# Kernel tuning notes

Hardware: AMD Instinct MI355X
Metric: run time of the kernel (lower is better)

Reference implementation:

```python
import jax, jax.numpy as jnp
import numpy as np

B, N, D = 8, 4096, 3
MAX_K = 16


def setup_inputs() -> dict:
    key = jax.random.key(0)
    k1, k2, k3 = jax.random.split(key, 3)
    x = jax.random.normal(k1, (B, N, D), dtype=jnp.float32)
    preds = jax.random.normal(k2, (B, N, D), dtype=jnp.float32)
    k_vector = jax.random.normal(k3, (MAX_K,), dtype=jnp.float32)  # learned param
    return {"x": x, "preds": preds, "k_vector": k_vector}


def _pairwise_dist(x):
    # Euclidean cdist via ||a||^2 + ||b||^2 - 2 a.b, avoiding a [B,N,N,D] tensor.
    sq = jnp.sum(x * x, axis=-1)                      # [B, N]
    inner = jnp.einsum('bnd,bmd->bnm', x, x)          # [B, N, N]
    d2 = sq[:, :, None] + sq[:, None, :] - 2.0 * inner
    return jnp.sqrt(jnp.maximum(d2, 0.0))             # [B, N, N]


def reference(x, preds, k_vector):
    # k = argmax(softmax(k_vector)) + 1 ; softmax is monotone so argmax suffices.
    # In the torch original .item() makes k a Python int (static w.r.t. the graph).
    k = int(np.asarray(jnp.argmax(k_vector))) + 1

    dist = _pairwise_dist(x)                          # [B, N, N]
    # torch.topk(..., largest=False): k smallest distances -> top_k of negated.
    _, idx = jax.lax.top_k(-dist, k)                  # idx: [B, N, k]

    # Gather predicted coords of the k nearest neighbors per point.
    b_idx = jnp.arange(preds.shape[0])[:, None, None]  # [B,1,1]
    knn_coords = preds[b_idx, idx]                     # [B, N, k, D]
    new_space = jnp.mean(knn_coords, axis=2)           # [B, N, D]
    return new_space
```

## Files before the change

kernel.cpp:

```cpp
#include <hip/hip_runtime.h>
#include <math.h>

typedef unsigned long long u64;
typedef unsigned int u32;

#define BB 8
#define NN 4096
#define MAXK 16
#define BQ 64
#define BUFSLOTS 16


__device__ __forceinline__ void bitonic16(u64 v[MAXK]) {
#pragma unroll
    for (int k = 2; k <= 16; k <<= 1) {
#pragma unroll
        for (int j = k >> 1; j > 0; j >>= 1) {
#pragma unroll
            for (int i = 0; i < 16; ++i) {
                const int l = i ^ j;
                if (l > i) {
                    const u64 a = v[i], b = v[l];
                    const bool up = ((i & k) == 0);
                    const bool sw = up ? (a > b) : (a < b);
                    v[i] = sw ? b : a;
                    v[l] = sw ? a : b;
                }
            }
        }
    }
}

__device__ __forceinline__ void merge16(u64 list[MAXK], const u64 br[MAXK]) {
    u64 lo[MAXK];
#pragma unroll
    for (int i = 0; i < 16; ++i) {
        const u64 a = list[i], b = br[15 - i];
        lo[i] = a < b ? a : b;
    }
#pragma unroll
    for (int j = 8; j > 0; j >>= 1) {
#pragma unroll
        for (int i = 0; i < 16; ++i) {
            const int l = i ^ j;
            if (l > i) {
                const u64 a = lo[i], b = lo[l];
                const bool sw = a > b;
                lo[i] = sw ? b : a;
                lo[l] = sw ? a : b;
            }
        }
    }
#pragma unroll
    for (int i = 0; i < 16; ++i) list[i] = lo[i];
}

__device__ __forceinline__ void flush_buf(u64 list[MAXK], u64& wkey, int& cnt,
                                          const u64 (*buf)[BQ], int lane) {
    u64 br[MAXK];
#pragma unroll
    for (int i = 0; i < 16; ++i) {
        const u64 v = buf[i][lane];
        br[i] = (i < cnt) ? v : ~0ull;
    }
    bitonic16(br);
    merge16(list, br);
    wkey = list[15];
    cnt = 0;
}

__device__ __forceinline__ void write_mean(const float* __restrict__ pb,
                                           const float* __restrict__ kvec,
                                           const u64 list[MAXK],
                                           float* __restrict__ op) {
    float bv = kvec[0]; int bi = 0;
#pragma unroll
    for (int i = 1; i < MAXK; ++i) { const float v = kvec[i]; if (v > bv) { bv = v; bi = i; } }
    const int k = bi + 1;
    float sx = 0.f, sy = 0.f, sz = 0.f;
#pragma unroll
    for (int s = 0; s < MAXK; ++s) {
        if (s < k) {
            const int j = (int)(u32)list[s];
            sx = __fadd_rn(sx, pb[j * 3 + 0]);
            sy = __fadd_rn(sy, pb[j * 3 + 1]);
            sz = __fadd_rn(sz, pb[j * 3 + 2]);
        }
    }
    const float fk = (float)k;
    op[0] = __fdiv_rn(sx, fk);
    op[1] = __fdiv_rn(sy, fk);
    op[2] = __fdiv_rn(sz, fk);
}

__global__ __launch_bounds__(256) void knn_prep(const float* __restrict__ x,
                                                float4* __restrict__ tab) {
    const int i = blockIdx.x * 256 + (int)threadIdx.x;
    const float cx = x[i * 3 + 0], cy = x[i * 3 + 1], cz = x[i * 3 + 2];
    const float sq = __fadd_rn(__fadd_rn(__fmul_rn(cx, cx), __fmul_rn(cy, cy)),
                               __fmul_rn(cz, cz));
    tab[i] = make_float4(cx, cy, cz, sq);
}

template <int SEGS, bool TAB, bool FUSED>
__global__ __launch_bounds__(BQ) void knn_scan(
    const float* __restrict__ x, const float* __restrict__ preds,
    const float* __restrict__ kvec, const float4* __restrict__ tab,
    u64* __restrict__ wkeys, float* __restrict__ out)
{
    constexpr int SEGLEN = NN / SEGS;
    int bid = blockIdx.x;
    const int seg = bid % SEGS;
    bid /= SEGS;
    const int qg = bid % (NN / BQ);
    const int b  = bid / (NN / BQ);
    const int lane = (int)threadIdx.x;
    const int qi = qg * BQ + lane;

    const float* xb = x + (size_t)b * NN * 3;
    const float4* tb = TAB ? (tab + (size_t)b * NN) : nullptr;

    float qx, qy, qz, qsq;
    if (TAB) {
        const float4 qv = tb[qi];
        qx = qv.x; qy = qv.y; qz = qv.z; qsq = qv.w;
    } else {
        qx = xb[qi * 3 + 0]; qy = xb[qi * 3 + 1]; qz = xb[qi * 3 + 2];
        qsq = __fadd_rn(__fadd_rn(__fmul_rn(qx, qx), __fmul_rn(qy, qy)),
                        __fmul_rn(qz, qz));
    }

    __shared__ u64 buf[BUFSLOTS][BQ];

    u64 list[MAXK];
#pragma unroll
    for (int s = 0; s < MAXK; ++s) list[s] = ~0ull;
    u64 wkey = ~0ull;
    int cnt = 0;

    const int jbase = seg * SEGLEN;
#pragma unroll 1
    for (int t = 0; t < SEGLEN; t += 4) {
        if (__any((int)(cnt > BUFSLOTS - 4))) flush_buf(list, wkey, cnt, buf, lane);
#pragma unroll
        for (int u = 0; u < 4; ++u) {
            const int j = jbase + t + u;
            float cx, cy, cz, csq;
            if (TAB) {
                const float4 c = tb[j];
                cx = c.x; cy = c.y; cz = c.z; csq = c.w;
            } else {
                cx = xb[j * 3 + 0]; cy = xb[j * 3 + 1]; cz = xb[j * 3 + 2];
                csq = __fadd_rn(__fadd_rn(__fmul_rn(cx, cx), __fmul_rn(cy, cy)),
                                __fmul_rn(cz, cz));
            }
            const float inner = __fadd_rn(
                __fadd_rn(__fmul_rn(qx, cx), __fmul_rn(qy, cy)),
                __fmul_rn(qz, cz));
            float d2 = __fsub_rn(__fadd_rn(qsq, csq), __fmul_rn(2.0f, inner));
            d2 = fmaxf(d2, 0.0f);
            const u64 key = ((u64)__float_as_uint(d2) << 32) | (u32)j;
            buf[cnt][lane] = key;
            cnt += (key < wkey) ? 1 : 0;
        }
    }
    flush_buf(list, wkey, cnt, buf, lane);

    if (FUSED) {
        write_mean(preds + (size_t)b * NN * 3, kvec, list,
                   out + ((size_t)b * NN + qi) * 3);
    } else {
        const size_t q = (size_t)b * NN + qi;
#pragma unroll
        for (int s = 0; s < MAXK; ++s)
            wkeys[(size_t)(seg * MAXK + s) * (BB * NN) + q] = list[s];
    }
}

template <int SEGS>
__global__ __launch_bounds__(BQ) void knn_merge(
    const float* __restrict__ preds, const float* __restrict__ kvec,
    const u64* __restrict__ wkeys, float* __restrict__ out)
{
    const int lane = (int)threadIdx.x;
    const int q = blockIdx.x * BQ + lane;

    __shared__ u64 buf[BUFSLOTS][BQ];

    u64 list[MAXK];
#pragma unroll
    for (int s = 0; s < MAXK; ++s) list[s] = ~0ull;
    u64 wkey = ~0ull;
    int cnt = 0;

#pragma unroll 1
    for (int i = 0; i < SEGS * MAXK; i += 4) {
        if (__any((int)(cnt > BUFSLOTS - 4))) flush_buf(list, wkey, cnt, buf, lane);
#pragma unroll
        for (int u = 0; u < 4; ++u) {
            const u64 key = wkeys[(size_t)(i + u) * (BB * NN) + q];
            buf[cnt][lane] = key;
            cnt += (key < wkey) ? 1 : 0;
        }
    }
    flush_buf(list, wkey, cnt, buf, lane);

    const int b = q / NN;
    write_mean(preds + (size_t)b * NN * 3, kvec, list, out + (size_t)q * 3);
}

extern "C" void kernel_launch(void* const* d_in, const int* in_sizes, int n_in,
                              void* d_out, int out_size, void* d_ws, size_t ws_size,
                              hipStream_t stream) {
    (void)in_sizes; (void)n_in; (void)out_size;
    const float* x     = (const float*)d_in[0];
    const float* preds = (const float*)d_in[1];
    const float* kvec  = (const float*)d_in[2];
    float* out = (float*)d_out;

    const size_t keys8 = 8ull * MAXK * BB * NN * sizeof(u64);
    const size_t keys4 = 4ull * MAXK * BB * NN * sizeof(u64);
    const size_t tabsz = (size_t)BB * NN * sizeof(float4);

    if (ws_size >= keys8 + tabsz) {
        u64* wkeys  = (u64*)d_ws;
        float4* tab = (float4*)((char*)d_ws + keys8);
        knn_prep<<<(BB * NN) / 256, 256, 0, stream>>>(x, tab);
        knn_scan<8, true, false><<<BB * (NN / BQ) * 8, BQ, 0, stream>>>(
            x, preds, kvec, tab, wkeys, out);
        knn_merge<8><<<(BB * NN) / BQ, BQ, 0, stream>>>(preds, kvec, wkeys, out);
    } else if (ws_size >= keys4 + tabsz) {
        u64* wkeys  = (u64*)d_ws;
        float4* tab = (float4*)((char*)d_ws + keys4);
        knn_prep<<<(BB * NN) / 256, 256, 0, stream>>>(x, tab);
        knn_scan<4, true, false><<<BB * (NN / BQ) * 4, BQ, 0, stream>>>(
            x, preds, kvec, tab, wkeys, out);
        knn_merge<4><<<(BB * NN) / BQ, BQ, 0, stream>>>(preds, kvec, wkeys, out);
    } else if (ws_size >= keys4) {
        u64* wkeys = (u64*)d_ws;
        knn_scan<4, false, false><<<BB * (NN / BQ) * 4, BQ, 0, stream>>>(
            x, preds, kvec, nullptr, wkeys, out);
        knn_merge<4><<<(BB * NN) / BQ, BQ, 0, stream>>>(preds, kvec, wkeys, out);
    } else {
        knn_scan<1, false, true><<<BB * (NN / BQ), BQ, 0, stream>>>(
            x, preds, kvec, nullptr, nullptr, out);
    }
}
```

Baseline: 158.5 us.

## Split KNN scan into 16 segments and merge sorted segment lists directly

The scan now splits candidates into 16 segments when the workspace allows, raising the number of blocks. The inner loop is unrolled to 8 candidates per buffer check. The prep table stores pre-doubled coordinates so the 2*inner multiply is dropped. The merge kernel runs with 256 threads and merges already-sorted 16-entry segment lists with merge16 instead of re-buffering and re-sorting every key. In exchange, the 16-way split writes and reads twice as many intermediate keys, and the larger buffer threshold causes more frequent flushes.

```diff
diff --git a/kernel.cpp b/kernel.cpp
--- a/kernel.cpp
+++ b/kernel.cpp
@@ -9,6 +9,7 @@
 #define MAXK 16
 #define BQ 64
 #define BUFSLOTS 16
+#define UNROLL 8
 
 
 __device__ __forceinline__ void bitonic16(u64 v[MAXK]) {
@@ -99,7 +100,8 @@
     const float cx = x[i * 3 + 0], cy = x[i * 3 + 1], cz = x[i * 3 + 2];
     const float sq = __fadd_rn(__fadd_rn(__fmul_rn(cx, cx), __fmul_rn(cy, cy)),
                                __fmul_rn(cz, cz));
-    tab[i] = make_float4(cx, cy, cz, sq);
+    tab[i] = make_float4(__fadd_rn(cx, cx), __fadd_rn(cy, cy),
+                         __fadd_rn(cz, cz), sq);
 }
 
 template <int SEGS, bool TAB, bool FUSED>
@@ -123,7 +125,10 @@
     float qx, qy, qz, qsq;
     if (TAB) {
         const float4 qv = tb[qi];
-        qx = qv.x; qy = qv.y; qz = qv.z; qsq = qv.w;
+        qx = __fmul_rn(0.5f, qv.x);
+        qy = __fmul_rn(0.5f, qv.y);
+        qz = __fmul_rn(0.5f, qv.z);
+        qsq = qv.w;
     } else {
         qx = xb[qi * 3 + 0]; qy = xb[qi * 3 + 1]; qz = xb[qi * 3 + 2];
         qsq = __fadd_rn(__fadd_rn(__fmul_rn(qx, qx), __fmul_rn(qy, qy)),
@@ -140,24 +145,25 @@
 
     const int jbase = seg * SEGLEN;
 #pragma unroll 1
-    for (int t = 0; t < SEGLEN; t += 4) {
-        if (__any((int)(cnt > BUFSLOTS - 4))) flush_buf(list, wkey, cnt, buf, lane);
-#pragma unroll
-        for (int u = 0; u < 4; ++u) {
+    for (int t = 0; t < SEGLEN; t += UNROLL) {
+        if (__any((int)(cnt > BUFSLOTS - UNROLL))) flush_buf(list, wkey, cnt, buf, lane);
+#pragma unroll
+        for (int u = 0; u < UNROLL; ++u) {
             const int j = jbase + t + u;
-            float cx, cy, cz, csq;
+            float c2x, c2y, c2z, csq;
             if (TAB) {
                 const float4 c = tb[j];
-                cx = c.x; cy = c.y; cz = c.z; csq = c.w;
+                c2x = c.x; c2y = c.y; c2z = c.z; csq = c.w;
             } else {
-                cx = xb[j * 3 + 0]; cy = xb[j * 3 + 1]; cz = xb[j * 3 + 2];
+                const float cx = xb[j * 3 + 0], cy = xb[j * 3 + 1], cz = xb[j * 3 + 2];
                 csq = __fadd_rn(__fadd_rn(__fmul_rn(cx, cx), __fmul_rn(cy, cy)),
                                 __fmul_rn(cz, cz));
+                c2x = __fadd_rn(cx, cx); c2y = __fadd_rn(cy, cy); c2z = __fadd_rn(cz, cz);
             }
-            const float inner = __fadd_rn(
-                __fadd_rn(__fmul_rn(qx, cx), __fmul_rn(qy, cy)),
-                __fmul_rn(qz, cz));
-            float d2 = __fsub_rn(__fadd_rn(qsq, csq), __fmul_rn(2.0f, inner));
+            const float inner2 = __fadd_rn(
+                __fadd_rn(__fmul_rn(qx, c2x), __fmul_rn(qy, c2y)),
+                __fmul_rn(qz, c2z));
+            float d2 = __fsub_rn(__fadd_rn(qsq, csq), inner2);
             d2 = fmaxf(d2, 0.0f);
             const u64 key = ((u64)__float_as_uint(d2) << 32) | (u32)j;
             buf[cnt][lane] = key;
@@ -178,32 +184,25 @@
 }
 
 template <int SEGS>
-__global__ __launch_bounds__(BQ) void knn_merge(
+__global__ __launch_bounds__(256) void knn_merge(
     const float* __restrict__ preds, const float* __restrict__ kvec,
     const u64* __restrict__ wkeys, float* __restrict__ out)
 {
-    const int lane = (int)threadIdx.x;
-    const int q = blockIdx.x * BQ + lane;
-
-    __shared__ u64 buf[BUFSLOTS][BQ];
+    const int q = blockIdx.x * 256 + (int)threadIdx.x;
 
     u64 list[MAXK];
 #pragma unroll
-    for (int s = 0; s < MAXK; ++s) list[s] = ~0ull;
-    u64 wkey = ~0ull;
-    int cnt = 0;
+    for (int s = 0; s < MAXK; ++s)
+        list[s] = wkeys[(size_t)s * (BB * NN) + q];
 
 #pragma unroll 1
-    for (int i = 0; i < SEGS * MAXK; i += 4) {
-        if (__any((int)(cnt > BUFSLOTS - 4))) flush_buf(list, wkey, cnt, buf, lane);
-#pragma unroll
-        for (int u = 0; u < 4; ++u) {
-            const u64 key = wkeys[(size_t)(i + u) * (BB * NN) + q];
-            buf[cnt][lane] = key;
-            cnt += (key < wkey) ? 1 : 0;
-        }
-    }
-    flush_buf(list, wkey, cnt, buf, lane);
+    for (int g = 1; g < SEGS; ++g) {
+        u64 br[MAXK];
+#pragma unroll
+        for (int s = 0; s < MAXK; ++s)
+            br[s] = wkeys[(size_t)(g * MAXK + s) * (BB * NN) + q];
+        merge16(list, br);
+    }
 
     const int b = q / NN;
     write_mean(preds + (size_t)b * NN * 3, kvec, list, out + (size_t)q * 3);
@@ -218,29 +217,30 @@
     const float* kvec  = (const float*)d_in[2];
     float* out = (float*)d_out;
 
-    const size_t keys8 = 8ull * MAXK * BB * NN * sizeof(u64);
-    const size_t keys4 = 4ull * MAXK * BB * NN * sizeof(u64);
-    const size_t tabsz = (size_t)BB * NN * sizeof(float4);
-
-    if (ws_size >= keys8 + tabsz) {
+    const size_t keys16 = 16ull * MAXK * BB * NN * sizeof(u64);
+    const size_t keys8  =  8ull * MAXK * BB * NN * sizeof(u64);
+    const size_t keys4  =  4ull * MAXK * BB * NN * sizeof(u64);
+    const size_t tabsz  = (size_t)BB * NN * sizeof(float4);
+
+    if (ws_size >= keys16 + tabsz) {
+        u64* wkeys  = (u64*)d_ws;
+        float4* tab = (float4*)((char*)d_ws + keys16);
+        knn_prep<<<(BB * NN) / 256, 256, 0, stream>>>(x, tab);
+        knn_scan<16, true, false><<<BB * (NN / BQ) * 16, BQ, 0, stream>>>(
+            x, preds, kvec, tab, wkeys, out);
+        knn_merge<16><<<(BB * NN) / 256, 256, 0, stream>>>(preds, kvec, wkeys, out);
+    } else if (ws_size >= keys8 + tabsz) {
         u64* wkeys  = (u64*)d_ws;
         float4* tab = (float4*)((char*)d_ws + keys8);
         knn_prep<<<(BB * NN) / 256, 256, 0, stream>>>(x, tab);
         knn_scan<8, true, false><<<BB * (NN / BQ) * 8, BQ, 0, stream>>>(
             x, preds, kvec, tab, wkeys, out);
-        knn_merge<8><<<(BB * NN) / BQ, BQ, 0, stream>>>(preds, kvec, wkeys, out);
-    } else if (ws_size >= keys4 + tabsz) {
-        u64* wkeys  = (u64*)d_ws;
-        float4* tab = (float4*)((char*)d_ws + keys4);
-        knn_prep<<<(BB * NN) / 256, 256, 0, stream>>>(x, tab);
-        knn_scan<4, true, false><<<BB * (NN / BQ) * 4, BQ, 0, stream>>>(
-            x, preds, kvec, tab, wkeys, out);
-        knn_merge<4><<<(BB * NN) / BQ, BQ, 0, stream>>>(preds, kvec, wkeys, out);
+        knn_merge<8><<<(BB * NN) / 256, 256, 0, stream>>>(preds, kvec, wkeys, out);
     } else if (ws_size >= keys4) {
         u64* wkeys = (u64*)d_ws;
         knn_scan<4, false, false><<<BB * (NN / BQ) * 4, BQ, 0, stream>>>(
             x, preds, kvec, nullptr, wkeys, out);
-        knn_merge<4><<<(BB * NN) / BQ, BQ, 0, stream>>>(preds, kvec, wkeys, out);
+        knn_merge<4><<<(BB * NN) / 256, 256, 0, stream>>>(preds, kvec, wkeys, out);
     } else {
         knn_scan<1, false, true><<<BB * (NN / BQ), BQ, 0, stream>>>(
             x, preds, kvec, nullptr, nullptr, out);
```

New measurement: 207.6 us. 1.31x slower.
